# Performance work log

Measured on AMD Instinct MI355X. Metric: run time of the kernel, lower is better.

Reference implementation:

```python
import jax, jax.numpy as jnp
import numpy as np

NUM_HEADS = 8
D_MODEL = 512
D_K = D_MODEL // NUM_HEADS


def setup_inputs() -> dict:
    key = jax.random.key(0)
    ks = jax.random.split(key, 8)
    B, C, L = 4, D_MODEL, 2048
    s = 1.0 / np.sqrt(C)  # xavier-ish scale for 1x1 convs
    return {
        "X_q": jax.random.normal(ks[0], (B, C, L), jnp.float32),
        "X_k": jax.random.normal(ks[1], (B, C, L), jnp.float32),
        "X_v": jax.random.normal(ks[2], (B, C, L), jnp.float32),
        "Wq": jax.random.normal(ks[3], (D_MODEL, C), jnp.float32) * s,
        "Wk": jax.random.normal(ks[4], (D_MODEL, C), jnp.float32) * s,
        "Wv": jax.random.normal(ks[5], (D_MODEL, C), jnp.float32) * s,
        "Wh": jax.random.normal(ks[6], (D_MODEL, D_MODEL), jnp.float32) * s,
        "bh": jnp.zeros((D_MODEL,), jnp.float32),
    }


def reference(X_q, X_k, X_v, Wq, Wk, Wv, Wh, bh):
    B, C, L = X_q.shape
    H, dk = NUM_HEADS, D_K

    def proj(x, W):  # 1x1 Conv1d, no bias: (B,Cin,L) -> (B,Cout,L)
        return jnp.einsum("oc,bcl->bol", W, x)

    # split_heads: (B, d_model, L) -> (B, H, d_k, L)
    Q = proj(X_q, Wq).reshape(B, H, dk, L)
    K = proj(X_k, Wk).reshape(B, H, dk, L)
    V = proj(X_v, Wv).reshape(B, H, dk, L)

    Q = Q / np.sqrt(dk).astype(np.float32)
    # scores: Q^T K -> (B, H, L_q, L_k)
    scores = jnp.einsum("bhdq,bhdk->bhqk", Q, K)
    A = jax.nn.softmax(scores, axis=-1)
    # H = A @ V^T -> (B, H, L, d_k); dropout is identity at eval
    Hh = jnp.einsum("bhqk,bhdk->bhqd", A, V)
    # group_heads: (B,H,L,dk) -> (B,H,dk,L) -> (B, d_model, L)
    H_cat = Hh.transpose(0, 1, 3, 2).reshape(B, H * dk, L)
    out = jnp.einsum("oc,bcl->bol", Wh, H_cat) + bh[None, :, None]
    return (out, A)
```

## Files before the change

kernel.cpp:

```cpp
#include <hip/hip_runtime.h>

#define L_SEQ 2048
#define CDIM  512
#define NB    4
#define NH    8
#define DKH   64

typedef __attribute__((ext_vector_type(8))) __bf16 bf16x8;
typedef __attribute__((ext_vector_type(4))) float  f32x4;
typedef __attribute__((ext_vector_type(8))) unsigned short u16x8;

__device__ __forceinline__ unsigned short f2bf(float f) {
  union { float f; unsigned u; } x; x.f = f;
  unsigned r = x.u + 0x7FFFu + ((x.u >> 16) & 1u);
  return (unsigned short)(r >> 16);
}
__device__ __forceinline__ float bf2f(unsigned short u) {
  union { unsigned u; float f; } x; x.u = ((unsigned)u) << 16;
  return x.f;
}
__device__ __forceinline__ bf16x8 ldfrag(const unsigned short* p) {
  u16x8 v = *reinterpret_cast<const u16x8*>(p);
  return __builtin_bit_cast(bf16x8, v);
}
__device__ __forceinline__ bf16x8 asbf(u16x8 v) { return __builtin_bit_cast(bf16x8, v); }
__device__ __forceinline__ float fexp2(float x) {
  float r; asm("v_exp_f32 %0, %1" : "=v"(r) : "v"(x)); return r;
}
#define MFMA(a,b,c) __builtin_amdgcn_mfma_f32_16x16x32_bf16((a),(b),(c),0,0,0)

__device__ __forceinline__ void loadset(u16x8* dst, const unsigned short* base,
                                        int kt, long stride) {
#pragma unroll
  for (int t = 0; t < 4; ++t) {
    const unsigned short* p = base + (size_t)(kt + t * 16) * stride;
    dst[2*t]   = *reinterpret_cast<const u16x8*>(p);
    dst[2*t+1] = *reinterpret_cast<const u16x8*>(p + 32);
  }
}
__device__ __forceinline__ void vloadset(u16x8* dst, const unsigned short* vbase,
                                         int kt) {
#pragma unroll
  for (int nt = 0; nt < 4; ++nt) {
    const unsigned short* vp = vbase + (size_t)(nt * 16) * L_SEQ + kt;
    dst[2*nt]   = *reinterpret_cast<const u16x8*>(vp);
    dst[2*nt+1] = *reinterpret_cast<const u16x8*>(vp + 32);
  }
}

__global__ __launch_bounds__(256) void k_cast(const float* __restrict__ X,
                                              unsigned short* __restrict__ Y, int n) {
  int i = (blockIdx.x * 256 + threadIdx.x) * 8;
  if (i + 8 > n) return;
  const float4* p = reinterpret_cast<const float4*>(X + i);
  float4 a = p[0], b = p[1];
  u16x8 o;
  o[0]=f2bf(a.x); o[1]=f2bf(a.y); o[2]=f2bf(a.z); o[3]=f2bf(a.w);
  o[4]=f2bf(b.x); o[5]=f2bf(b.y); o[6]=f2bf(b.z); o[7]=f2bf(b.w);
  *reinterpret_cast<u16x8*>(Y + i) = o;
}

__global__ __launch_bounds__(256) void k_transpose(const float* __restrict__ X,
                                                   unsigned short* __restrict__ Xt) {
  __shared__ __align__(16) unsigned short t[64][72];
  int l0 = blockIdx.x * 64, c0 = blockIdx.y * 64;
  size_t boff = (size_t)blockIdx.z * CDIM * L_SEQ;
  const float* Xb = X + boff;
  unsigned short* Xtb = Xt + boff;
  int tid = threadIdx.x;
  int cc = tid >> 2, lo = (tid & 3) * 16;
  const float* src = Xb + (size_t)(c0 + cc) * L_SEQ + l0 + lo;
#pragma unroll
  for (int i = 0; i < 4; ++i) {
    float4 v = *reinterpret_cast<const float4*>(src + i * 4);
    t[lo + i*4 + 0][cc] = f2bf(v.x);
    t[lo + i*4 + 1][cc] = f2bf(v.y);
    t[lo + i*4 + 2][cc] = f2bf(v.z);
    t[lo + i*4 + 3][cc] = f2bf(v.w);
  }
  __syncthreads();
  int ll = tid >> 2, co = (tid & 3) * 16;
  unsigned short* dst = Xtb + (size_t)(l0 + ll) * CDIM + c0 + co;
  u16x8 a = *reinterpret_cast<const u16x8*>(&t[ll][co]);
  u16x8 b = *reinterpret_cast<const u16x8*>(&t[ll][co + 8]);
  *reinterpret_cast<u16x8*>(dst) = a;
  *reinterpret_cast<u16x8*>(dst + 8) = b;
}

template<int OUT_BF16, int HAS_BIAS>
__global__ __launch_bounds__(256) void k_gemm_nt(
    const unsigned short* __restrict__ A, long sA,
    const unsigned short* __restrict__ Bt, long sB,
    void* __restrict__ Out, long sO,
    const float* __restrict__ bias, float scale, int M, int N) {
  __shared__ __align__(16) unsigned short lA[128 * 64];
  __shared__ __align__(16) unsigned short lB[128 * 64];
  int b = blockIdx.z;
  const unsigned short* Ab = A + (size_t)b * sA;
  const unsigned short* Bb = Bt + (size_t)b * sB;
  int m0 = blockIdx.y * 128, n0 = blockIdx.x * 128;
  int tid = threadIdx.x, lane = tid & 63, wave = tid >> 6;
  int wm = (wave >> 1) * 64, wn = (wave & 1) * 64;
  f32x4 acc[4][4] = {};
  int srow = tid >> 3;
  int sslot = tid & 7;

  for (int k0 = 0; k0 < 512; k0 += 64) {
    __syncthreads();
#pragma unroll
    for (int i = 0; i < 4; ++i) {
      int r = srow + 32 * i;
      int sw = (sslot ^ (r & 7)) * 8;
      u16x8 va = *reinterpret_cast<const u16x8*>(Ab + (size_t)(m0 + r) * 512 + k0 + sslot * 8);
      *reinterpret_cast<u16x8*>(&lA[r * 64 + sw]) = va;
      u16x8 vb = *reinterpret_cast<const u16x8*>(Bb + (size_t)(n0 + r) * 512 + k0 + sslot * 8);
      *reinterpret_cast<u16x8*>(&lB[r * 64 + sw]) = vb;
    }
    __syncthreads();
#pragma unroll
    for (int c = 0; c < 2; ++c) {
      bf16x8 af[4], bfr[4];
#pragma unroll
      for (int t = 0; t < 4; ++t) {
        int ra = wm + t * 16 + (lane & 15);
        int sa = (lane >> 4) + 4 * c;
        af[t] = ldfrag(&lA[ra * 64 + ((sa ^ (ra & 7)) * 8)]);
        int rb = wn + t * 16 + (lane & 15);
        bfr[t] = ldfrag(&lB[rb * 64 + ((sa ^ (rb & 7)) * 8)]);
      }
#pragma unroll
      for (int i = 0; i < 4; ++i)
#pragma unroll
        for (int j = 0; j < 4; ++j)
          acc[i][j] = MFMA(af[i], bfr[j], acc[i][j]);
    }
  }
  int row4 = (lane >> 4) * 4, col = lane & 15;
#pragma unroll
  for (int i = 0; i < 4; ++i)
#pragma unroll
    for (int j = 0; j < 4; ++j)
#pragma unroll
      for (int e = 0; e < 4; ++e) {
        int r = m0 + wm + i * 16 + row4 + e;
        int cN = n0 + wn + j * 16 + col;
        float v = acc[i][j][e] * scale;
        if (HAS_BIAS) v += bias[r];
        size_t idx = (size_t)b * sO + (size_t)r * N + cN;
        if (OUT_BF16) ((unsigned short*)Out)[idx] = f2bf(v);
        else          ((float*)Out)[idx] = v;
      }
}

__global__ __launch_bounds__(256) void k_attn(
    const unsigned short* __restrict__ Qt,
    const unsigned short* __restrict__ Kt,
    const unsigned short* __restrict__ Vn,
    unsigned short* __restrict__ HhT,
    float* __restrict__ Aout) {
  __shared__ __align__(16) unsigned short al[4][1024];
  int bh = blockIdx.y;
  int b = bh >> 3, h = bh & 7;
  int lane = threadIdx.x & 63, wave = threadIdx.x >> 6;
  int q0 = blockIdx.x * 64 + wave * 16;
  const unsigned short* Qh = Qt + (size_t)b * L_SEQ * CDIM + h * DKH;
  const unsigned short* Kh = Kt + (size_t)b * L_SEQ * CDIM + h * DKH;
  const unsigned short* Vh = Vn + (size_t)b * CDIM * L_SEQ + (size_t)h * DKH * L_SEQ;
  unsigned short* Ho = HhT + (size_t)b * L_SEQ * CDIM + h * DKH;
  float* Ab = Aout + (size_t)bh * L_SEQ * L_SEQ;

  int fr = lane & 15, fg = lane >> 4;
  bf16x8 qf0 = ldfrag(Qh + (size_t)(q0 + fr) * CDIM + fg * 8);
  bf16x8 qf1 = ldfrag(Qh + (size_t)(q0 + fr) * CDIM + fg * 8 + 32);

  const unsigned short* kbase = Kh + (size_t)fr * CDIM + fg * 8;
  const unsigned short* vbase = Vh + (size_t)fr * L_SEQ + fg * 8;

  float psum[4] = {0.f, 0.f, 0.f, 0.f};
  {
    u16x8 ka[8], kb2[8];
    auto half1 = [&](const u16x8* ks) {
#pragma unroll
      for (int t = 0; t < 4; ++t) {
        f32x4 s = {0.f, 0.f, 0.f, 0.f};
        s = MFMA(qf0, asbf(ks[2*t]), s);
        s = MFMA(qf1, asbf(ks[2*t+1]), s);
#pragma unroll
        for (int e = 0; e < 4; ++e) psum[e] += fexp2(s[e]);
      }
    };
    loadset(ka, kbase, 0, CDIM);
    for (int i = 0; i < 32; i += 2) {
      loadset(kb2, kbase, (i + 1) * 64, CDIM);
      half1(ka);
      loadset(ka, kbase, ((i + 2) & 31) * 64, CDIM);
      half1(kb2);
    }
  }
#pragma unroll
  for (int e = 0; e < 4; ++e) {
    psum[e] += __shfl_xor(psum[e], 1, 64);
    psum[e] += __shfl_xor(psum[e], 2, 64);
    psum[e] += __shfl_xor(psum[e], 4, 64);
    psum[e] += __shfl_xor(psum[e], 8, 64);
  }
  float inv[4];
#pragma unroll
  for (int e = 0; e < 4; ++e) inv[e] = 1.0f / psum[e];

  f32x4 oacc[4] = {};
  unsigned short* alw = al[wave];
  {
    u16x8 ka[8], kb2[8], va[8], vb2[8];
    auto half2 = [&](const u16x8* ks, const u16x8* vs, int kt) {
#pragma unroll
      for (int t = 0; t < 4; ++t) {
        f32x4 s = {0.f, 0.f, 0.f, 0.f};
        s = MFMA(qf0, asbf(ks[2*t]), s);
        s = MFMA(qf1, asbf(ks[2*t+1]), s);
#pragma unroll
        for (int e = 0; e < 4; ++e) {
          float a = fexp2(s[e]) * inv[e];
          int row = fg * 4 + e;
          int byte = (row * 128 + (t * 16 + fr) * 2) ^ ((row & 7) << 4);
          alw[byte >> 1] = f2bf(a);
        }
      }
      int byA0 = (fr * 128 + fg * 16) ^ ((fr & 7) << 4);
      int byA1 = (fr * 128 + (fg + 4) * 16) ^ ((fr & 7) << 4);
      bf16x8 af0 = ldfrag(alw + (byA0 >> 1));
      bf16x8 af1 = ldfrag(alw + (byA1 >> 1));
#pragma unroll
      for (int nt = 0; nt < 4; ++nt) {
        oacc[nt] = MFMA(af0, asbf(vs[2*nt]), oacc[nt]);
        oacc[nt] = MFMA(af1, asbf(vs[2*nt+1]), oacc[nt]);
      }
      {
        int wrow = lane >> 2;
        int slot0 = (lane & 3) * 2;
        int by0 = (wrow * 128 + slot0 * 16) ^ ((wrow & 7) << 4);
        int by1 = (wrow * 128 + (slot0 + 1) * 16) ^ ((wrow & 7) << 4);
        u16x8 p0 = *reinterpret_cast<const u16x8*>(alw + (by0 >> 1));
        u16x8 p1 = *reinterpret_cast<const u16x8*>(alw + (by1 >> 1));
        float* dp = Ab + (size_t)(q0 + wrow) * L_SEQ + kt + (lane & 3) * 16;
        f32x4 f0 = {bf2f(p0[0]), bf2f(p0[1]), bf2f(p0[2]), bf2f(p0[3])};
        f32x4 f1 = {bf2f(p0[4]), bf2f(p0[5]), bf2f(p0[6]), bf2f(p0[7])};
        f32x4 f2 = {bf2f(p1[0]), bf2f(p1[1]), bf2f(p1[2]), bf2f(p1[3])};
        f32x4 f3 = {bf2f(p1[4]), bf2f(p1[5]), bf2f(p1[6]), bf2f(p1[7])};
        *reinterpret_cast<f32x4*>(dp + 0)  = f0;
        *reinterpret_cast<f32x4*>(dp + 4)  = f1;
        *reinterpret_cast<f32x4*>(dp + 8)  = f2;
        *reinterpret_cast<f32x4*>(dp + 12) = f3;
      }
    };
    loadset(ka, kbase, 0, CDIM);
    vloadset(va, vbase, 0);
    for (int i = 0; i < 32; i += 2) {
      loadset(kb2, kbase, (i + 1) * 64, CDIM);
      vloadset(vb2, vbase, (i + 1) * 64);
      half2(ka, va, i * 64);
      loadset(ka, kbase, ((i + 2) & 31) * 64, CDIM);
      vloadset(va, vbase, ((i + 2) & 31) * 64);
      half2(kb2, vb2, (i + 1) * 64);
    }
  }
#pragma unroll
  for (int nt = 0; nt < 4; ++nt)
#pragma unroll
    for (int e = 0; e < 4; ++e)
      Ho[(size_t)(q0 + fg * 4 + e) * CDIM + nt * 16 + fr] = f2bf(oacc[nt][e]);
}

extern "C" void kernel_launch(void* const* d_in, const int* in_sizes, int n_in,
                              void* d_out, int out_size, void* d_ws, size_t ws_size,
                              hipStream_t stream) {
  const float* Xq = (const float*)d_in[0];
  const float* Xk = (const float*)d_in[1];
  const float* Xv = (const float*)d_in[2];
  const float* Wq = (const float*)d_in[3];
  const float* Wk = (const float*)d_in[4];
  const float* Wv = (const float*)d_in[5];
  const float* Wh = (const float*)d_in[6];
  const float* bh = (const float*)d_in[7];

  const size_t PROJ = (size_t)NB * L_SEQ * CDIM;
  float* out_f = (float*)d_out;
  float* A_out = out_f + PROJ;

  unsigned short* Qt = (unsigned short*)d_out;
  unsigned short* Kt = Qt + PROJ;
  unsigned short* Xtq = (unsigned short*)A_out;
  unsigned short* Xtk = Xtq + PROJ;
  unsigned short* Xtv = Xtk + PROJ;
  unsigned short* Vn  = (unsigned short*)d_ws;
  unsigned short* HhT = Vn + PROJ;
  unsigned short* Wqb = HhT + PROJ;
  unsigned short* Wkb = Wqb + CDIM * CDIM;
  unsigned short* Wvb = Wkb + CDIM * CDIM;
  unsigned short* Whb = Wvb + CDIM * CDIM;

  int nW = CDIM * CDIM;
  k_cast<<<nW / 2048, 256, 0, stream>>>(Wq, Wqb, nW);
  k_cast<<<nW / 2048, 256, 0, stream>>>(Wk, Wkb, nW);
  k_cast<<<nW / 2048, 256, 0, stream>>>(Wv, Wvb, nW);
  k_cast<<<nW / 2048, 256, 0, stream>>>(Wh, Whb, nW);

  dim3 tg(L_SEQ / 64, CDIM / 64, NB);
  k_transpose<<<tg, 256, 0, stream>>>(Xq, Xtq);
  k_transpose<<<tg, 256, 0, stream>>>(Xk, Xtk);
  k_transpose<<<tg, 256, 0, stream>>>(Xv, Xtv);

  const long sLC = (long)L_SEQ * CDIM;
  k_gemm_nt<1, 0><<<dim3(CDIM / 128, L_SEQ / 128, NB), 256, 0, stream>>>(
      Xtq, sLC, Wqb, 0, Qt, sLC, nullptr, 0.18033688f, L_SEQ, CDIM);
  k_gemm_nt<1, 0><<<dim3(CDIM / 128, L_SEQ / 128, NB), 256, 0, stream>>>(
      Xtk, sLC, Wkb, 0, Kt, sLC, nullptr, 1.0f, L_SEQ, CDIM);
  k_gemm_nt<1, 0><<<dim3(L_SEQ / 128, CDIM / 128, NB), 256, 0, stream>>>(
      Wvb, 0, Xtv, sLC, Vn, sLC, nullptr, 1.0f, CDIM, L_SEQ);

  k_attn<<<dim3(L_SEQ / 64, NB * NH), 256, 0, stream>>>(Qt, Kt, Vn, HhT, A_out);

  k_gemm_nt<0, 1><<<dim3(L_SEQ / 128, CDIM / 128, NB), 256, 0, stream>>>(
      Whb, 0, HhT, sLC, out_f, sLC, bh, 1.0f, CDIM, L_SEQ);
}
```

Before: 527.2 us.

## Use single-wave attention blocks with XCD-aware head mapping and simpler loops

The attention kernel now runs one 64-thread wave per block instead of four waves per 256-thread block. The block index is remapped so that all blocks of a given (batch, head) land on the same XCD (nbid & 7), which is meant to improve L2 reuse of K and V. The manual double-buffered register prefetch of K and V tiles is replaced by a simple per-iteration load, which lowers register pressure but relies on occupancy rather than explicit prefetch to hide latency. The A-matrix write is also moved ahead of the PV MFMA.

```diff
diff --git a/kernel.cpp b/kernel.cpp
--- a/kernel.cpp
+++ b/kernel.cpp
@@ -152,17 +152,20 @@
       }
 }
 
-__global__ __launch_bounds__(256) void k_attn(
+__global__ __launch_bounds__(64) void k_attn(
     const unsigned short* __restrict__ Qt,
     const unsigned short* __restrict__ Kt,
     const unsigned short* __restrict__ Vn,
     unsigned short* __restrict__ HhT,
     float* __restrict__ Aout) {
-  __shared__ __align__(16) unsigned short al[4][1024];
-  int bh = blockIdx.y;
+  __shared__ __align__(16) unsigned short al[1024];
+  int nbid = blockIdx.y * gridDim.x + blockIdx.x;
+  int xcd = nbid & 7, slot = nbid >> 3;
+  int bh = xcd * 4 + (slot >> 7);
+  int qt = slot & 127;
   int b = bh >> 3, h = bh & 7;
-  int lane = threadIdx.x & 63, wave = threadIdx.x >> 6;
-  int q0 = blockIdx.x * 64 + wave * 16;
+  int lane = threadIdx.x;
+  int q0 = qt * 16;
   const unsigned short* Qh = Qt + (size_t)b * L_SEQ * CDIM + h * DKH;
   const unsigned short* Kh = Kt + (size_t)b * L_SEQ * CDIM + h * DKH;
   const unsigned short* Vh = Vn + (size_t)b * CDIM * L_SEQ + (size_t)h * DKH * L_SEQ;
@@ -177,24 +180,16 @@
   const unsigned short* vbase = Vh + (size_t)fr * L_SEQ + fg * 8;
 
   float psum[4] = {0.f, 0.f, 0.f, 0.f};
-  {
-    u16x8 ka[8], kb2[8];
-    auto half1 = [&](const u16x8* ks) {
-#pragma unroll
-      for (int t = 0; t < 4; ++t) {
-        f32x4 s = {0.f, 0.f, 0.f, 0.f};
-        s = MFMA(qf0, asbf(ks[2*t]), s);
-        s = MFMA(qf1, asbf(ks[2*t+1]), s);
-#pragma unroll
-        for (int e = 0; e < 4; ++e) psum[e] += fexp2(s[e]);
-      }
-    };
-    loadset(ka, kbase, 0, CDIM);
-    for (int i = 0; i < 32; i += 2) {
-      loadset(kb2, kbase, (i + 1) * 64, CDIM);
-      half1(ka);
-      loadset(ka, kbase, ((i + 2) & 31) * 64, CDIM);
-      half1(kb2);
+  for (int i = 0; i < 32; ++i) {
+    u16x8 kr[8];
+    loadset(kr, kbase, i * 64, CDIM);
+#pragma unroll
+    for (int t = 0; t < 4; ++t) {
+      f32x4 s = {0.f, 0.f, 0.f, 0.f};
+      s = MFMA(qf0, asbf(kr[2*t]), s);
+      s = MFMA(qf1, asbf(kr[2*t+1]), s);
+#pragma unroll
+      for (int e = 0; e < 4; ++e) psum[e] += fexp2(s[e]);
     }
   }
 #pragma unroll
@@ -209,59 +204,49 @@
   for (int e = 0; e < 4; ++e) inv[e] = 1.0f / psum[e];
 
   f32x4 oacc[4] = {};
-  unsigned short* alw = al[wave];
-  {
-    u16x8 ka[8], kb2[8], va[8], vb2[8];
-    auto half2 = [&](const u16x8* ks, const u16x8* vs, int kt) {
-#pragma unroll
-      for (int t = 0; t < 4; ++t) {
-        f32x4 s = {0.f, 0.f, 0.f, 0.f};
-        s = MFMA(qf0, asbf(ks[2*t]), s);
-        s = MFMA(qf1, asbf(ks[2*t+1]), s);
-#pragma unroll
-        for (int e = 0; e < 4; ++e) {
-          float a = fexp2(s[e]) * inv[e];
-          int row = fg * 4 + e;
-          int byte = (row * 128 + (t * 16 + fr) * 2) ^ ((row & 7) << 4);
-          alw[byte >> 1] = f2bf(a);
-        }
+  for (int i = 0; i < 32; ++i) {
+    int kt = i * 64;
+    u16x8 kr[8], vr[8];
+    loadset(kr, kbase, kt, CDIM);
+    vloadset(vr, vbase, kt);
+#pragma unroll
+    for (int t = 0; t < 4; ++t) {
+      f32x4 s = {0.f, 0.f, 0.f, 0.f};
+      s = MFMA(qf0, asbf(kr[2*t]), s);
+      s = MFMA(qf1, asbf(kr[2*t+1]), s);
+#pragma unroll
+      for (int e = 0; e < 4; ++e) {
+        float a = fexp2(s[e]) * inv[e];
+        int row = fg * 4 + e;
+        int byte = (row * 128 + (t * 16 + fr) * 2) ^ ((row & 7) << 4);
+        al[byte >> 1] = f2bf(a);
       }
-      int byA0 = (fr * 128 + fg * 16) ^ ((fr & 7) << 4);
-      int byA1 = (fr * 128 + (fg + 4) * 16) ^ ((fr & 7) << 4);
-      bf16x8 af0 = ldfrag(alw + (byA0 >> 1));
-      bf16x8 af1 = ldfrag(alw + (byA1 >> 1));
-#pragma unroll
-      for (int nt = 0; nt < 4; ++nt) {
-        oacc[nt] = MFMA(af0, asbf(vs[2*nt]), oacc[nt]);
-        oacc[nt] = MFMA(af1, asbf(vs[2*nt+1]), oacc[nt]);
-      }
-      {
-        int wrow = lane >> 2;
-        int slot0 = (lane & 3) * 2;
-        int by0 = (wrow * 128 + slot0 * 16) ^ ((wrow & 7) << 4);
-        int by1 = (wrow * 128 + (slot0 + 1) * 16) ^ ((wrow & 7) << 4);
-        u16x8 p0 = *reinterpret_cast<const u16x8*>(alw + (by0 >> 1));
-        u16x8 p1 = *reinterpret_cast<const u16x8*>(alw + (by1 >> 1));
-        float* dp = Ab + (size_t)(q0 + wrow) * L_SEQ + kt + (lane & 3) * 16;
-        f32x4 f0 = {bf2f(p0[0]), bf2f(p0[1]), bf2f(p0[2]), bf2f(p0[3])};
-        f32x4 f1 = {bf2f(p0[4]), bf2f(p0[5]), bf2f(p0[6]), bf2f(p0[7])};
-        f32x4 f2 = {bf2f(p1[0]), bf2f(p1[1]), bf2f(p1[2]), bf2f(p1[3])};
-        f32x4 f3 = {bf2f(p1[4]), bf2f(p1[5]), bf2f(p1[6]), bf2f(p1[7])};
-        *reinterpret_cast<f32x4*>(dp + 0)  = f0;
-        *reinterpret_cast<f32x4*>(dp + 4)  = f1;
-        *reinterpret_cast<f32x4*>(dp + 8)  = f2;
-        *reinterpret_cast<f32x4*>(dp + 12) = f3;
-      }
-    };
-    loadset(ka, kbase, 0, CDIM);
-    vloadset(va, vbase, 0);
-    for (int i = 0; i < 32; i += 2) {
-      loadset(kb2, kbase, (i + 1) * 64, CDIM);
-      vloadset(vb2, vbase, (i + 1) * 64);
-      half2(ka, va, i * 64);
-      loadset(ka, kbase, ((i + 2) & 31) * 64, CDIM);
-      vloadset(va, vbase, ((i + 2) & 31) * 64);
-      half2(kb2, vb2, (i + 1) * 64);
+    }
+    {
+      int wrow = lane >> 2;
+      int slot0 = (lane & 3) * 2;
+      int by0 = (wrow * 128 + slot0 * 16) ^ ((wrow & 7) << 4);
+      int by1 = (wrow * 128 + (slot0 + 1) * 16) ^ ((wrow & 7) << 4);
+      u16x8 p0 = *reinterpret_cast<const u16x8*>(al + (by0 >> 1));
+      u16x8 p1 = *reinterpret_cast<const u16x8*>(al + (by1 >> 1));
+      float* dp = Ab + (size_t)(q0 + wrow) * L_SEQ + kt + (lane & 3) * 16;
+      f32x4 f0 = {bf2f(p0[0]), bf2f(p0[1]), bf2f(p0[2]), bf2f(p0[3])};
+      f32x4 f1 = {bf2f(p0[4]), bf2f(p0[5]), bf2f(p0[6]), bf2f(p0[7])};
+      f32x4 f2 = {bf2f(p1[0]), bf2f(p1[1]), bf2f(p1[2]), bf2f(p1[3])};
+      f32x4 f3 = {bf2f(p1[4]), bf2f(p1[5]), bf2f(p1[6]), bf2f(p1[7])};
+      *reinterpret_cast<f32x4*>(dp + 0)  = f0;
+      *reinterpret_cast<f32x4*>(dp + 4)  = f1;
+      *reinterpret_cast<f32x4*>(dp + 8)  = f2;
+      *reinterpret_cast<f32x4*>(dp + 12) = f3;
+    }
+    int byA0 = (fr * 128 + fg * 16) ^ ((fr & 7) << 4);
+    int byA1 = (fr * 128 + (fg + 4) * 16) ^ ((fr & 7) << 4);
+    bf16x8 af0 = ldfrag(al + (byA0 >> 1));
+    bf16x8 af1 = ldfrag(al + (byA1 >> 1));
+#pragma unroll
+    for (int nt = 0; nt < 4; ++nt) {
+      oacc[nt] = MFMA(af0, asbf(vr[2*nt]), oacc[nt]);
+      oacc[nt] = MFMA(af1, asbf(vr[2*nt+1]), oacc[nt]);
     }
   }
 #pragma unroll
@@ -318,7 +303,7 @@
   k_gemm_nt<1, 0><<<dim3(L_SEQ / 128, CDIM / 128, NB), 256, 0, stream>>>(
       Wvb, 0, Xtv, sLC, Vn, sLC, nullptr, 1.0f, CDIM, L_SEQ);
 
-  k_attn<<<dim3(L_SEQ / 64, NB * NH), 256, 0, stream>>>(Qt, Kt, Vn, HhT, A_out);
+  k_attn<<<dim3(128, 32), 64, 0, stream>>>(Qt, Kt, Vn, HhT, A_out);
 
   k_gemm_nt<0, 1><<<dim3(L_SEQ / 128, CDIM / 128, NB), 256, 0, stream>>>(
       Whb, 0, HhT, sLC, out_f, sLC, bh, 1.0f, CDIM, L_SEQ);
```

After: 522.7 us. About the same (-0.9%).
